# Kernel tuning notes

Hardware: AMD Instinct MI355X
Metric: run time of the kernel (lower is better)

The kernel has to match this reference:

```python
import jax, jax.numpy as jnp
import numpy as np

B, T, D, H = 2, 2048, 1024, 16
STD = 0.02

def setup_inputs() -> dict:
    key = jax.random.key(0)
    ks = jax.random.split(key, 5)
    x = jax.random.normal(ks[0], (B, T, D), dtype=jnp.float32)
    Wq = jax.random.normal(ks[1], (D, D), dtype=jnp.float32) * STD
    Wk = jax.random.normal(ks[2], (D, D), dtype=jnp.float32) * STD
    Wv = jax.random.normal(ks[3], (D, D), dtype=jnp.float32) * STD
    Wo = jax.random.normal(ks[4], (D, D), dtype=jnp.float32) * STD
    z = jnp.zeros((D,), dtype=jnp.float32)
    return {"x": x, "Wq": Wq, "bq": z, "Wk": Wk, "bk": z, "Wv": Wv, "bv": z, "Wo": Wo, "bo": z}

def _split(t, h):
    b, s, dm = t.shape
    return t.reshape(b, s, h, dm // h).transpose(0, 2, 1, 3)  # (B,h,T,d)

def reference(x, Wq, bq, Wk, bk, Wv, bv, Wo, bo):
    h = H
    # linear projections (nn.Linear: y = x @ W^T + b)
    q = _split(x @ Wq.T + bq, h)
    k = _split(x @ Wk.T + bk, h)
    v = _split(x @ Wv.T + bv, h)
    d_k = k.shape[-1]
    # scaled dot-product similarities (B,h,T,T)
    sim = jnp.einsum("bhqd,bhkd->bhqk", q, k) / jnp.sqrt(jnp.float32(d_k))
    # causal mask: upper triangle (excluding diag) filled with -inf
    Tq = sim.shape[-1]
    causal = jnp.tril(jnp.ones((Tq, Tq), dtype=bool))
    sim = jnp.where(causal, sim, -jnp.inf)
    attn = jax.nn.softmax(sim, axis=-1)
    ctx = jnp.einsum("bhqk,bhkd->bhqd", attn, v)  # (B,h,T,d)
    ctx = ctx.transpose(0, 2, 1, 3).reshape(x.shape[0], x.shape[1], -1)  # (B,T,D)
    return ctx @ Wo.T + bo
```

## Files before the change

### kernel.cpp

```cpp
#include <hip/hip_runtime.h>
#include <hip/hip_bf16.h>


typedef __attribute__((ext_vector_type(8))) short bf16x8;
typedef __attribute__((ext_vector_type(4))) float f32x4;
typedef __attribute__((ext_vector_type(4))) short s16x4;

#define QSCALE 0.18033688011f

__constant__ int QTA[20] = {11,10,9,8,15,15,7,14,14,13,13,6,12,12,5,4,3,2,1,0};
__constant__ int HFA[20] = {-1,-1,-1,-1,0,1,-1,0,1,0,1,-1,0,1,-1,-1,-1,-1,-1,-1};

__device__ __forceinline__ int sniff_f32(const void* p) {
    const unsigned short* u = (const unsigned short*)p;
    int c = 0;
    for (int i = 0; i < 256; ++i) {
        int e = (u[i] >> 7) & 0xFF;
        c += (e >= 0x90) ? 1 : 0;
    }
    return c > 8;
}

__device__ __forceinline__ void async_copy16(const void* g, void* l) {
    __builtin_amdgcn_global_load_lds(
        (const __attribute__((address_space(1))) void*)g,
        (__attribute__((address_space(3))) void*)l, 16, 0, 0);
}

struct Cvt { const void* src; __hip_bfloat16* dst; int n; };
struct CvtPack { Cvt a[9]; };

__global__ __launch_bounds__(256) void cvt_bf16(CvtPack pk) {
    const Cvt c = pk.a[blockIdx.y];
    const int f32 = sniff_f32(c.src);
    const int stride = gridDim.x * 256 * 8;
    for (int idx = (blockIdx.x * 256 + threadIdx.x) * 8; idx < c.n; idx += stride) {
        if (f32) {
            const float* s = (const float*)c.src + idx;
            f32x4 a0 = *(const f32x4*)s;
            f32x4 a1 = *(const f32x4*)(s + 4);
            union { __hip_bfloat16 h[8]; bf16x8 v; } u;
#pragma unroll
            for (int e = 0; e < 4; e++) u.h[e]     = (__hip_bfloat16)a0[e];
#pragma unroll
            for (int e = 0; e < 4; e++) u.h[4 + e] = (__hip_bfloat16)a1[e];
            *(bf16x8*)&c.dst[idx] = u.v;
        } else {
            *(bf16x8*)&c.dst[idx] = *(const bf16x8*)((const __hip_bfloat16*)c.src + idx);
        }
    }
}

template <int MODE>
__device__ __forceinline__ void gemm_async_body(
    const __hip_bfloat16* __restrict__ A, const __hip_bfloat16* __restrict__ W,
    const __hip_bfloat16* __restrict__ bias, void* __restrict__ C,
    int M, int N, int K, int bm, int bn, float outscale,
    __hip_bfloat16* smem)
{
    const int tid  = threadIdx.x;
    const int wave = tid >> 6;
    const int lane = tid & 63;
    const int quad = lane >> 4;
    const int l15  = lane & 15;
    const int wr   = wave >> 1;
    const int wc   = wave & 1;

    const int srow = wave * 16 + (lane >> 2);
    const int scol = (lane & 3) * 8;
    const __hip_bfloat16* gA0 = A + (size_t)(bm + srow) * K + scol;
    const __hip_bfloat16* gB0 = W + (size_t)(bn + srow) * K + scol;

    f32x4 acc[4][4];
#pragma unroll
    for (int i = 0; i < 4; i++)
#pragma unroll
        for (int j = 0; j < 4; j++) acc[i][j] = (f32x4)0.0f;

#define QSTAGE(buf, k0) { \
        __hip_bfloat16* d_ = smem + (buf) * 8192 + wave * 512; \
        async_copy16(gA0 + (k0), d_); \
        async_copy16(gA0 + (size_t)64 * K + (k0), d_ + 2048); \
        async_copy16(gB0 + (k0), d_ + 4096); \
        async_copy16(gB0 + (size_t)64 * K + (k0), d_ + 4096 + 2048); \
    }

    const int nt = K >> 5;
    QSTAGE(0, 0);
    for (int t = 0; t < nt; ++t) {
        const int buf = t & 1;
        const __hip_bfloat16* sA = smem + buf * 8192;
        const __hip_bfloat16* sB = sA + 4096;
        if (t + 1 < nt) {
            QSTAGE(1 - buf, (t + 1) * 32);
            asm volatile("s_waitcnt vmcnt(4)" ::: "memory");
        } else {
            asm volatile("s_waitcnt vmcnt(0)" ::: "memory");
        }
        __builtin_amdgcn_s_barrier();

        bf16x8 af[4], bf[4];
#pragma unroll
        for (int i = 0; i < 4; i++)
            af[i] = *(const bf16x8*)&sA[(wr * 64 + i * 16 + l15) * 32 + quad * 8];
#pragma unroll
        for (int j = 0; j < 4; j++)
            bf[j] = *(const bf16x8*)&sB[(wc * 64 + j * 16 + l15) * 32 + quad * 8];
#pragma unroll
        for (int i = 0; i < 4; i++)
#pragma unroll
            for (int j = 0; j < 4; j++)
                acc[i][j] = __builtin_amdgcn_mfma_f32_16x16x32_bf16(af[i], bf[j], acc[i][j], 0, 0, 0);

        __builtin_amdgcn_s_barrier();
    }
#undef QSTAGE

    float bv[4];
#pragma unroll
    for (int j = 0; j < 4; j++)
        bv[j] = (float)bias[bn + wc * 64 + j * 16 + l15];

    if (MODE == 2) {
        __hip_bfloat16* sOut = smem;
        __syncthreads();
#pragma unroll
        for (int i = 0; i < 4; i++) {
            int tl = wr * 64 + i * 16 + quad * 4;
#pragma unroll
            for (int j = 0; j < 4; j++) {
                int dl = wc * 64 + j * 16 + l15;
                union { __hip_bfloat16 e[4]; s16x4 v; } u;
#pragma unroll
                for (int r = 0; r < 4; r++)
                    u.e[r] = (__hip_bfloat16)(acc[i][j][r] + bv[j]);
                *(s16x4*)&sOut[dl * 136 + tl] = u.v;
            }
        }
        __syncthreads();
        __hip_bfloat16* VTo = (__hip_bfloat16*)C;
        const int bb = bm >> 11, tt0 = bm & 2047;
#pragma unroll
        for (int g8 = 0; g8 < 8; g8++) {
            int idx = g8 * 256 + tid;
            int dl  = idx >> 4;
            int tc  = (idx & 15) * 8;
            int dg  = bn + dl;
            bf16x8 v = *(const bf16x8*)&sOut[dl * 136 + tc];
            *(bf16x8*)&VTo[(((size_t)bb * 16 + (dg >> 6)) * 64 + (dg & 63)) * 2048 + tt0 + tc] = v;
        }
    } else {
#pragma unroll
        for (int i = 0; i < 4; i++) {
#pragma unroll
            for (int j = 0; j < 4; j++) {
                int col = bn + wc * 64 + j * 16 + l15;
#pragma unroll
                for (int r = 0; r < 4; r++) {
                    int row = bm + wr * 64 + i * 16 + quad * 4 + r;
                    float v = (acc[i][j][r] + bv[j]) * outscale;
                    if (MODE == 1) ((float*)C)[(size_t)row * N + col] = v;
                    else ((__hip_bfloat16*)C)[(size_t)row * N + col] = (__hip_bfloat16)v;
                }
            }
        }
    }
}

__global__ __launch_bounds__(256, 2) void qkv_gemm(
    const __hip_bfloat16* __restrict__ x,
    const __hip_bfloat16* __restrict__ Wq, const __hip_bfloat16* __restrict__ bq, __hip_bfloat16* __restrict__ Q,
    const __hip_bfloat16* __restrict__ Wk, const __hip_bfloat16* __restrict__ bk, __hip_bfloat16* __restrict__ Kb,
    const __hip_bfloat16* __restrict__ Wv, const __hip_bfloat16* __restrict__ bv, __hip_bfloat16* __restrict__ VT,
    int M, int N, int K)
{
    __shared__ __hip_bfloat16 smem[128 * 136];
    if (blockIdx.z == 0)
        gemm_async_body<0>(x, Wq, bq, Q, M, N, K, blockIdx.x * 128, blockIdx.y * 128, QSCALE, smem);
    else if (blockIdx.z == 1)
        gemm_async_body<0>(x, Wk, bk, Kb, M, N, K, blockIdx.x * 128, blockIdx.y * 128, 1.0f, smem);
    else
        gemm_async_body<2>(x, Wv, bv, VT, M, N, K, blockIdx.x * 128, blockIdx.y * 128, 1.0f, smem);
}

template <bool OF32>
__device__ __forceinline__ void gemm64_body(
    const __hip_bfloat16* __restrict__ A, const __hip_bfloat16* __restrict__ W,
    const __hip_bfloat16* __restrict__ bias, void* __restrict__ C,
    int M, int N, int K, int bm, int bn,
    __hip_bfloat16* smem)
{
    const int tid  = threadIdx.x;
    const int wave = tid >> 6;
    const int lane = tid & 63;
    const int quad = lane >> 4;
    const int l15  = lane & 15;

    const int srow = wave * 16 + (lane >> 2);
    const int scol = (lane & 3) * 8;
    const __hip_bfloat16* gA0 = A + (size_t)(bm + srow) * K + scol;
    const __hip_bfloat16* gB0 = W + (size_t)(bn + srow) * K + scol;

    f32x4 acc[4][2];
#pragma unroll
    for (int i = 0; i < 4; i++)
#pragma unroll
        for (int j = 0; j < 2; j++) acc[i][j] = (f32x4)0.0f;

#define OSTAGE(buf, k0) { \
        __hip_bfloat16* d_ = smem + (buf) * 6144; \
        async_copy16(gA0 + (k0), d_ + wave * 512); \
        async_copy16(gB0 + (k0), d_ + 2048 + wave * 512); \
        async_copy16(gB0 + (size_t)64 * K + (k0), d_ + 2048 + wave * 512 + 2048); \
    }

    const int nt = K >> 5;
    OSTAGE(0, 0);
    for (int t = 0; t < nt; ++t) {
        const int buf = t & 1;
        const __hip_bfloat16* sA = smem + buf * 6144;
        const __hip_bfloat16* sB = sA + 2048;
        if (t + 1 < nt) {
            OSTAGE(1 - buf, (t + 1) * 32);
            asm volatile("s_waitcnt vmcnt(3)" ::: "memory");
        } else {
            asm volatile("s_waitcnt vmcnt(0)" ::: "memory");
        }
        __builtin_amdgcn_s_barrier();

        bf16x8 af[4], bf[2];
#pragma unroll
        for (int i = 0; i < 4; i++)
            af[i] = *(const bf16x8*)&sA[(i * 16 + l15) * 32 + quad * 8];
#pragma unroll
        for (int j = 0; j < 2; j++)
            bf[j] = *(const bf16x8*)&sB[(wave * 32 + j * 16 + l15) * 32 + quad * 8];
#pragma unroll
        for (int i = 0; i < 4; i++)
#pragma unroll
            for (int j = 0; j < 2; j++)
                acc[i][j] = __builtin_amdgcn_mfma_f32_16x16x32_bf16(af[i], bf[j], acc[i][j], 0, 0, 0);

        __builtin_amdgcn_s_barrier();
    }
#undef OSTAGE

    float bv[2];
#pragma unroll
    for (int j = 0; j < 2; j++)
        bv[j] = (float)bias[bn + wave * 32 + j * 16 + l15];
#pragma unroll
    for (int i = 0; i < 4; i++) {
#pragma unroll
        for (int j = 0; j < 2; j++) {
            int col = bn + wave * 32 + j * 16 + l15;
#pragma unroll
            for (int r = 0; r < 4; r++) {
                int row = bm + i * 16 + quad * 4 + r;
                float v = acc[i][j][r] + bv[j];
                if (OF32) ((float*)C)[(size_t)row * N + col] = v;
                else      ((__hip_bfloat16*)C)[(size_t)row * N + col] = (__hip_bfloat16)v;
            }
        }
    }
}

__global__ __launch_bounds__(256, 2) void out_gemm(
    const __hip_bfloat16* __restrict__ A, const __hip_bfloat16* __restrict__ W,
    const __hip_bfloat16* __restrict__ bias, const void* __restrict__ origW,
    void* __restrict__ C, int M, int N, int K)
{
    __shared__ __hip_bfloat16 smem[2 * 6144];
    __shared__ int f32flag;
    if (threadIdx.x == 0) f32flag = sniff_f32(origW);
    __syncthreads();
    if (f32flag)
        gemm64_body<true>(A, W, bias, C, M, N, K, blockIdx.x * 64, blockIdx.y * 128, smem);
    else
        gemm64_body<false>(A, W, bias, C, M, N, K, blockIdx.x * 64, blockIdx.y * 128, smem);
}

#define PAD 68

__global__ __launch_bounds__(512, 3) void attn_causal(
    const __hip_bfloat16* __restrict__ Q,
    const __hip_bfloat16* __restrict__ K,
    const __hip_bfloat16* __restrict__ VT,
    __hip_bfloat16* __restrict__ O,
    float* __restrict__ PO, float* __restrict__ PL,
    int T, int D, int H)
{
    __shared__ __hip_bfloat16 sK[2][64 * PAD];
    __shared__ __hip_bfloat16 sVT[2][64 * PAD];
    __shared__ __hip_bfloat16 sPA[8][16 * PAD];

    const int tid  = threadIdx.x;
    const int wave = tid >> 6;
    const int lane = tid & 63;
    const int quad = lane >> 4;
    const int l15  = lane & 15;

    const int srow = tid >> 3;
    const int sc8  = (tid & 7) * 8;

    const int rank = blockIdx.x >> 5;
    const int hb   = blockIdx.x & 31;
    const int h    = hb & 15;
    const int b    = hb >> 4;
    const int qt   = QTA[rank];
    const int hf   = HFA[rank];
    const int nkt  = 2 * qt + 2;
    const int mid  = qt + 1;
    const int kt0  = (hf == 1) ? mid : 0;
    const int kt1  = (hf == 0) ? mid : nkt;

    const size_t headoff = (size_t)b * T * D + (size_t)h * 64;
    const size_t vtoff   = ((size_t)b * H + h) * 64 * (size_t)T;
    const int qbase    = qt * 128 + wave * 16;
    const int myrowmax = qbase + 15;

    bf16x8 qfrag[2];
#pragma unroll
    for (int kk = 0; kk < 2; kk++)
        qfrag[kk] = *(const bf16x8*)&Q[headoff +
            (size_t)(qbase + l15) * D + kk * 32 + quad * 8];

    f32x4 acc_o[4];
#pragma unroll
    for (int j = 0; j < 4; j++) acc_o[j] = (f32x4)0.0f;
    float lacc = 0.f;

    bf16x8 pk, pv;
    pk = *(const bf16x8*)&K[headoff + (size_t)(kt0 * 64 + srow) * D + sc8];
    pv = *(const bf16x8*)&VT[vtoff + (size_t)srow * T + kt0 * 64 + sc8];
    *(bf16x8*)&sK[0][srow * PAD + sc8]  = pk;
    *(bf16x8*)&sVT[0][srow * PAD + sc8] = pv;
    if (kt0 + 1 < kt1) {
        pk = *(const bf16x8*)&K[headoff + (size_t)((kt0 + 1) * 64 + srow) * D + sc8];
        pv = *(const bf16x8*)&VT[vtoff + (size_t)srow * T + (kt0 + 1) * 64 + sc8];
    }
    __syncthreads();

    for (int kt = kt0; kt < kt1; ++kt) {
        const int cur = (kt - kt0) & 1;

        if (kt + 1 < kt1) {
            *(bf16x8*)&sK[1 - cur][srow * PAD + sc8]  = pk;
            *(bf16x8*)&sVT[1 - cur][srow * PAD + sc8] = pv;
            if (kt + 2 < kt1) {
                pk = *(const bf16x8*)&K[headoff + (size_t)((kt + 2) * 64 + srow) * D + sc8];
                pv = *(const bf16x8*)&VT[vtoff + (size_t)srow * T + (kt + 2) * 64 + sc8];
            }
        }

        if (kt * 64 <= myrowmax) {
            bf16x8 kfrag[2][4], vfrag[2][4];
#pragma unroll
            for (int kk = 0; kk < 2; kk++)
#pragma unroll
                for (int j = 0; j < 4; j++) {
                    kfrag[kk][j] = *(const bf16x8*)&sK[cur][(j * 16 + l15) * PAD + kk * 32 + quad * 8];
                    vfrag[kk][j] = *(const bf16x8*)&sVT[cur][(j * 16 + l15) * PAD + kk * 32 + quad * 8];
                }

            f32x4 st[4];
#pragma unroll
            for (int j = 0; j < 4; j++) st[j] = (f32x4)0.0f;
            __builtin_amdgcn_s_setprio(1);
#pragma unroll
            for (int kk = 0; kk < 2; kk++)
#pragma unroll
                for (int j = 0; j < 4; j++)
                    st[j] = __builtin_amdgcn_mfma_f32_16x16x32_bf16(
                        kfrag[kk][j], qfrag[kk], st[j], 0, 0, 0);
            __builtin_amdgcn_s_setprio(0);

            if (kt * 64 + 63 > qbase) {
                const int q = qbase + l15;
#pragma unroll
                for (int j = 0; j < 4; j++) {
                    int keyb = kt * 64 + j * 16 + quad * 4;
#pragma unroll
                    for (int r = 0; r < 4; r++)
                        if (keyb + r > q) st[j][r] = -1e30f;
                }
            }

#pragma unroll
            for (int j = 0; j < 4; j++) {
                union { __hip_bfloat16 e[4]; s16x4 v; } u;
#pragma unroll
                for (int r = 0; r < 4; r++) {
                    float p = exp2f(st[j][r]);
                    lacc += p;
                    u.e[r] = (__hip_bfloat16)p;
                }
                *(s16x4*)&sPA[wave][l15 * PAD + j * 16 + quad * 4] = u.v;
            }
            __builtin_amdgcn_s_setprio(1);
#pragma unroll
            for (int kk = 0; kk < 2; kk++) {
                bf16x8 a = *(const bf16x8*)&sPA[wave][l15 * PAD + kk * 32 + quad * 8];
#pragma unroll
                for (int j = 0; j < 4; j++)
                    acc_o[j] = __builtin_amdgcn_mfma_f32_16x16x32_bf16(
                        a, vfrag[kk][j], acc_o[j], 0, 0, 0);
            }
            __builtin_amdgcn_s_setprio(0);
        }

        __syncthreads();
    }

    lacc += __shfl_xor(lacc, 16, 64);
    lacc += __shfl_xor(lacc, 32, 64);

    if (hf >= 0) {
        const int pidx = (((b * 16 + h) * 4) + (qt - 12)) * 2 + hf;
        float* POt = PO + (size_t)pidx * 8192;
#pragma unroll
        for (int r = 0; r < 4; r++) {
            int rl = wave * 16 + quad * 4 + r;
#pragma unroll
            for (int j = 0; j < 4; j++)
                POt[rl * 64 + j * 16 + l15] = acc_o[j][r];
        }
        if (quad == 0) PL[pidx * 128 + wave * 16 + l15] = lacc;
    } else {
#pragma unroll
        for (int r = 0; r < 4; r++) {
            float linv = 1.0f / __shfl(lacc, quad * 4 + r, 64);
            int row = qbase + quad * 4 + r;
#pragma unroll
            for (int j = 0; j < 4; j++) {
                int col = j * 16 + l15;
                O[headoff + (size_t)row * D + col] = (__hip_bfloat16)(acc_o[j][r] * linv);
            }
        }
    }
}

__global__ __launch_bounds__(256) void attn_combine(
    const float* __restrict__ PO, const float* __restrict__ PL,
    __hip_bfloat16* __restrict__ O, int T, int D, int H)
{
    const int tix = blockIdx.x;
    const int qt  = 12 + (tix & 3);
    const int h   = (tix >> 2) & 15;
    const int b   = tix >> 6;
    const float* P0 = PO + (size_t)(2 * tix) * 8192;
    const float* P1 = P0 + 8192;
    const float* L0 = PL + 2 * tix * 128;
    const float* L1 = L0 + 128;
    const size_t headoff = (size_t)b * T * D + (size_t)h * 64;
    const int rowbase = qt * 128;

    for (int e = threadIdx.x; e < 8192; e += 256) {
        int rr = e >> 6, cc = e & 63;
        float linv = 1.0f / (L0[rr] + L1[rr]);
        float v = (P0[e] + P1[e]) * linv;
        O[headoff + (size_t)(rowbase + rr) * D + cc] = (__hip_bfloat16)v;
    }
}

extern "C" void kernel_launch(void* const* d_in, const int* in_sizes, int n_in,
                              void* d_out, int out_size, void* d_ws, size_t ws_size,
                              hipStream_t stream) {
    const int Bb = 2, T = 2048, D = 1024, H = 16;
    const int M = Bb * T;

    __hip_bfloat16* w = (__hip_bfloat16*)d_ws;
    __hip_bfloat16* Q   = w;
    __hip_bfloat16* Kb  = Q   + (size_t)M * D;
    __hip_bfloat16* VT  = Kb  + (size_t)M * D;
    __hip_bfloat16* ctx = VT  + (size_t)M * D;
    __hip_bfloat16* xb  = ctx + (size_t)M * D;
    __hip_bfloat16* Wqb = xb  + (size_t)M * D;
    __hip_bfloat16* Wkb = Wqb + (size_t)D * D;
    __hip_bfloat16* Wvb = Wkb + (size_t)D * D;
    __hip_bfloat16* Wob = Wvb + (size_t)D * D;
    __hip_bfloat16* bqb = Wob + (size_t)D * D;
    __hip_bfloat16* bkb = bqb + D;
    __hip_bfloat16* bvb = bkb + D;
    __hip_bfloat16* bob = bvb + D;

    float* PO = (float*)xb;
    float* PL = (float*)Wqb;

    CvtPack pk;
    pk.a[0] = { d_in[0], xb,  M * D };
    pk.a[1] = { d_in[1], Wqb, D * D };
    pk.a[2] = { d_in[2], bqb, D };
    pk.a[3] = { d_in[3], Wkb, D * D };
    pk.a[4] = { d_in[4], bkb, D };
    pk.a[5] = { d_in[5], Wvb, D * D };
    pk.a[6] = { d_in[6], bvb, D };
    pk.a[7] = { d_in[7], Wob, D * D };
    pk.a[8] = { d_in[8], bob, D };

    cvt_bf16<<<dim3(512, 9), 256, 0, stream>>>(pk);
    qkv_gemm<<<dim3(M / 128, D / 128, 3), 256, 0, stream>>>(
        xb, Wqb, bqb, Q, Wkb, bkb, Kb, Wvb, bvb, VT, M, D, D);
    attn_causal<<<dim3(640, 1, 1), 512, 0, stream>>>(
        Q, Kb, VT, ctx, PO, PL, T, D, H);
    attn_combine<<<dim3(128, 1, 1), 256, 0, stream>>>(PO, PL, ctx, T, D, H);
    out_gemm<<<dim3(M / 64, D / 128), 256, 0, stream>>>(
        ctx, Wob, bob, d_in[7], d_out, M, D, D);
}
```

Before: 212.5 us.

## Process 32 query rows per wave in causal attention with 4-wave blocks

The attention kernel now runs 4 waves of 256 threads instead of 8, and each wave handles two 16-row query groups. The K/V fragments loaded from LDS are reused across both groups, which halves the LDS fragment reads per query row. Each thread also stages two rows of the K/V tiles. The cost is higher register pressure from doubled accumulators and Q fragments, fewer waves per block to hide latency, and coarser causal skipping, since a wave only skips a tile when both of its groups are fully masked.

New measurement: 248.8 us. +17.1%, slower.

```diff
diff --git a/kernel.cpp b/kernel.cpp
--- a/kernel.cpp
+++ b/kernel.cpp
@@ -282,7 +282,7 @@
 
 #define PAD 68
 
-__global__ __launch_bounds__(512, 3) void attn_causal(
+__global__ __launch_bounds__(256, 3) void attn_causal(
     const __hip_bfloat16* __restrict__ Q,
     const __hip_bfloat16* __restrict__ K,
     const __hip_bfloat16* __restrict__ VT,
@@ -292,7 +292,7 @@
 {
     __shared__ __hip_bfloat16 sK[2][64 * PAD];
     __shared__ __hip_bfloat16 sVT[2][64 * PAD];
-    __shared__ __hip_bfloat16 sPA[8][16 * PAD];
+    __shared__ __hip_bfloat16 sPA[4][32 * PAD];
 
     const int tid  = threadIdx.x;
     const int wave = tid >> 6;
@@ -316,28 +316,44 @@
 
     const size_t headoff = (size_t)b * T * D + (size_t)h * 64;
     const size_t vtoff   = ((size_t)b * H + h) * 64 * (size_t)T;
-    const int qbase    = qt * 128 + wave * 16;
-    const int myrowmax = qbase + 15;
-
-    bf16x8 qfrag[2];
-#pragma unroll
-    for (int kk = 0; kk < 2; kk++)
-        qfrag[kk] = *(const bf16x8*)&Q[headoff +
-            (size_t)(qbase + l15) * D + kk * 32 + quad * 8];
-
-    f32x4 acc_o[4];
-#pragma unroll
-    for (int j = 0; j < 4; j++) acc_o[j] = (f32x4)0.0f;
-    float lacc = 0.f;
-
-    bf16x8 pk, pv;
-    pk = *(const bf16x8*)&K[headoff + (size_t)(kt0 * 64 + srow) * D + sc8];
-    pv = *(const bf16x8*)&VT[vtoff + (size_t)srow * T + kt0 * 64 + sc8];
-    *(bf16x8*)&sK[0][srow * PAD + sc8]  = pk;
-    *(bf16x8*)&sVT[0][srow * PAD + sc8] = pv;
+    const int qbase    = qt * 128 + wave * 32;
+    const int myrowmax = qbase + 31;
+
+    bf16x8 qfrag[2][2];
+#pragma unroll
+    for (int g = 0; g < 2; g++)
+#pragma unroll
+        for (int kk = 0; kk < 2; kk++)
+            qfrag[g][kk] = *(const bf16x8*)&Q[headoff +
+                (size_t)(qbase + g * 16 + l15) * D + kk * 32 + quad * 8];
+
+    f32x4 acc_o[2][4];
+#pragma unroll
+    for (int g = 0; g < 2; g++)
+#pragma unroll
+        for (int j = 0; j < 4; j++) acc_o[g][j] = (f32x4)0.0f;
+    float lacc[2] = {0.f, 0.f};
+
+    bf16x8 pk[2], pv[2];
+#pragma unroll
+    for (int u = 0; u < 2; u++) {
+        int row = srow + u * 32;
+        pk[u] = *(const bf16x8*)&K[headoff + (size_t)(kt0 * 64 + row) * D + sc8];
+        pv[u] = *(const bf16x8*)&VT[vtoff + (size_t)row * T + kt0 * 64 + sc8];
+    }
+#pragma unroll
+    for (int u = 0; u < 2; u++) {
+        int row = srow + u * 32;
+        *(bf16x8*)&sK[0][row * PAD + sc8]  = pk[u];
+        *(bf16x8*)&sVT[0][row * PAD + sc8] = pv[u];
+    }
     if (kt0 + 1 < kt1) {
-        pk = *(const bf16x8*)&K[headoff + (size_t)((kt0 + 1) * 64 + srow) * D + sc8];
-        pv = *(const bf16x8*)&VT[vtoff + (size_t)srow * T + (kt0 + 1) * 64 + sc8];
+#pragma unroll
+        for (int u = 0; u < 2; u++) {
+            int row = srow + u * 32;
+            pk[u] = *(const bf16x8*)&K[headoff + (size_t)((kt0 + 1) * 64 + row) * D + sc8];
+            pv[u] = *(const bf16x8*)&VT[vtoff + (size_t)row * T + (kt0 + 1) * 64 + sc8];
+        }
     }
     __syncthreads();
 
@@ -345,11 +361,19 @@
         const int cur = (kt - kt0) & 1;
 
         if (kt + 1 < kt1) {
-            *(bf16x8*)&sK[1 - cur][srow * PAD + sc8]  = pk;
-            *(bf16x8*)&sVT[1 - cur][srow * PAD + sc8] = pv;
+#pragma unroll
+            for (int u = 0; u < 2; u++) {
+                int row = srow + u * 32;
+                *(bf16x8*)&sK[1 - cur][row * PAD + sc8]  = pk[u];
+                *(bf16x8*)&sVT[1 - cur][row * PAD + sc8] = pv[u];
+            }
             if (kt + 2 < kt1) {
-                pk = *(const bf16x8*)&K[headoff + (size_t)((kt + 2) * 64 + srow) * D + sc8];
-                pv = *(const bf16x8*)&VT[vtoff + (size_t)srow * T + (kt + 2) * 64 + sc8];
+#pragma unroll
+                for (int u = 0; u < 2; u++) {
+                    int row = srow + u * 32;
+                    pk[u] = *(const bf16x8*)&K[headoff + (size_t)((kt + 2) * 64 + row) * D + sc8];
+                    pv[u] = *(const bf16x8*)&VT[vtoff + (size_t)row * T + (kt + 2) * 64 + sc8];
+                }
             }
         }
 
@@ -363,80 +387,94 @@
                     vfrag[kk][j] = *(const bf16x8*)&sVT[cur][(j * 16 + l15) * PAD + kk * 32 + quad * 8];
                 }
 
-            f32x4 st[4];
-#pragma unroll
-            for (int j = 0; j < 4; j++) st[j] = (f32x4)0.0f;
+#pragma unroll
+            for (int g = 0; g < 2; g++) {
+                const int qb = qbase + g * 16;
+                f32x4 st[4];
+#pragma unroll
+                for (int j = 0; j < 4; j++) st[j] = (f32x4)0.0f;
+                __builtin_amdgcn_s_setprio(1);
+#pragma unroll
+                for (int kk = 0; kk < 2; kk++)
+#pragma unroll
+                    for (int j = 0; j < 4; j++)
+                        st[j] = __builtin_amdgcn_mfma_f32_16x16x32_bf16(
+                            kfrag[kk][j], qfrag[g][kk], st[j], 0, 0, 0);
+                __builtin_amdgcn_s_setprio(0);
+
+                if (kt * 64 + 63 > qb) {
+                    const int q = qb + l15;
+#pragma unroll
+                    for (int j = 0; j < 4; j++) {
+                        int keyb = kt * 64 + j * 16 + quad * 4;
+#pragma unroll
+                        for (int r = 0; r < 4; r++)
+                            if (keyb + r > q) st[j][r] = -1e30f;
+                    }
+                }
+
+#pragma unroll
+                for (int j = 0; j < 4; j++) {
+                    union { __hip_bfloat16 e[4]; s16x4 v; } u;
+#pragma unroll
+                    for (int r = 0; r < 4; r++) {
+                        float p = exp2f(st[j][r]);
+                        lacc[g] += p;
+                        u.e[r] = (__hip_bfloat16)p;
+                    }
+                    *(s16x4*)&sPA[wave][(g * 16 + l15) * PAD + j * 16 + quad * 4] = u.v;
+                }
+            }
             __builtin_amdgcn_s_setprio(1);
 #pragma unroll
-            for (int kk = 0; kk < 2; kk++)
-#pragma unroll
-                for (int j = 0; j < 4; j++)
-                    st[j] = __builtin_amdgcn_mfma_f32_16x16x32_bf16(
-                        kfrag[kk][j], qfrag[kk], st[j], 0, 0, 0);
+            for (int g = 0; g < 2; g++)
+#pragma unroll
+                for (int kk = 0; kk < 2; kk++) {
+                    bf16x8 a = *(const bf16x8*)&sPA[wave][(g * 16 + l15) * PAD + kk * 32 + quad * 8];
+#pragma unroll
+                    for (int j = 0; j < 4; j++)
+                        acc_o[g][j] = __builtin_amdgcn_mfma_f32_16x16x32_bf16(
+                            a, vfrag[kk][j], acc_o[g][j], 0, 0, 0);
+                }
             __builtin_amdgcn_s_setprio(0);
-
-            if (kt * 64 + 63 > qbase) {
-                const int q = qbase + l15;
-#pragma unroll
-                for (int j = 0; j < 4; j++) {
-                    int keyb = kt * 64 + j * 16 + quad * 4;
-#pragma unroll
-                    for (int r = 0; r < 4; r++)
-                        if (keyb + r > q) st[j][r] = -1e30f;
-                }
-            }
-
-#pragma unroll
-            for (int j = 0; j < 4; j++) {
-                union { __hip_bfloat16 e[4]; s16x4 v; } u;
-#pragma unroll
-                for (int r = 0; r < 4; r++) {
-                    float p = exp2f(st[j][r]);
-                    lacc += p;
-                    u.e[r] = (__hip_bfloat16)p;
-                }
-                *(s16x4*)&sPA[wave][l15 * PAD + j * 16 + quad * 4] = u.v;
-            }
-            __builtin_amdgcn_s_setprio(1);
-#pragma unroll
-            for (int kk = 0; kk < 2; kk++) {
-                bf16x8 a = *(const bf16x8*)&sPA[wave][l15 * PAD + kk * 32 + quad * 8];
-#pragma unroll
-                for (int j = 0; j < 4; j++)
-                    acc_o[j] = __builtin_amdgcn_mfma_f32_16x16x32_bf16(
-                        a, vfrag[kk][j], acc_o[j], 0, 0, 0);
-            }
-            __builtin_amdgcn_s_setprio(0);
         }
 
         __syncthreads();
     }
 
-    lacc += __shfl_xor(lacc, 16, 64);
-    lacc += __shfl_xor(lacc, 32, 64);
+#pragma unroll
+    for (int g = 0; g < 2; g++) {
+        lacc[g] += __shfl_xor(lacc[g], 16, 64);
+        lacc[g] += __shfl_xor(lacc[g], 32, 64);
+    }
 
     if (hf >= 0) {
         const int pidx = (((b * 16 + h) * 4) + (qt - 12)) * 2 + hf;
         float* POt = PO + (size_t)pidx * 8192;
 #pragma unroll
-        for (int r = 0; r < 4; r++) {
-            int rl = wave * 16 + quad * 4 + r;
-#pragma unroll
-            for (int j = 0; j < 4; j++)
-                POt[rl * 64 + j * 16 + l15] = acc_o[j][r];
-        }
-        if (quad == 0) PL[pidx * 128 + wave * 16 + l15] = lacc;
+        for (int g = 0; g < 2; g++) {
+#pragma unroll
+            for (int r = 0; r < 4; r++) {
+                int rl = wave * 32 + g * 16 + quad * 4 + r;
+#pragma unroll
+                for (int j = 0; j < 4; j++)
+                    POt[rl * 64 + j * 16 + l15] = acc_o[g][j][r];
+            }
+            if (quad == 0) PL[pidx * 128 + wave * 32 + g * 16 + l15] = lacc[g];
+        }
     } else {
 #pragma unroll
-        for (int r = 0; r < 4; r++) {
-            float linv = 1.0f / __shfl(lacc, quad * 4 + r, 64);
-            int row = qbase + quad * 4 + r;
-#pragma unroll
-            for (int j = 0; j < 4; j++) {
-                int col = j * 16 + l15;
-                O[headoff + (size_t)row * D + col] = (__hip_bfloat16)(acc_o[j][r] * linv);
-            }
-        }
+        for (int g = 0; g < 2; g++)
+#pragma unroll
+            for (int r = 0; r < 4; r++) {
+                float linv = 1.0f / __shfl(lacc[g], quad * 4 + r, 64);
+                int row = qbase + g * 16 + quad * 4 + r;
+#pragma unroll
+                for (int j = 0; j < 4; j++) {
+                    int col = j * 16 + l15;
+                    O[headoff + (size_t)row * D + col] = (__hip_bfloat16)(acc_o[g][j][r] * linv);
+                }
+            }
     }
 }
 
@@ -501,7 +539,7 @@
     cvt_bf16<<<dim3(512, 9), 256, 0, stream>>>(pk);
     qkv_gemm<<<dim3(M / 128, D / 128, 3), 256, 0, stream>>>(
         xb, Wqb, bqb, Q, Wkb, bkb, Kb, Wvb, bvb, VT, M, D, D);
-    attn_causal<<<dim3(640, 1, 1), 512, 0, stream>>>(
+    attn_causal<<<dim3(640, 1, 1), 256, 0, stream>>>(
         Q, Kb, VT, ctx, PO, PL, T, D, H);
     attn_combine<<<dim3(128, 1, 1), 256, 0, stream>>>(PO, PL, ctx, T, D, H);
     out_gemm<<<dim3(M / 64, D / 128), 256, 0, stream>>>(
```
